# Optimization experiments

Measured on AMD Instinct MI355X. Metric: run time of the kernel, lower is better.

## Reference

```python
import jax, jax.numpy as jnp
import numpy as np

# geomloss SamplesLoss('sinkhorn', p=2, blur=0.05, diameter=4.0, scaling=0.5, debias=True)
P_EXP = 2.0
BLUR = 0.05
DIAMETER = 4.0
SCALING = 0.5


def eps_schedule():
    # geomloss epsilon_schedule: annealed temperatures from diameter^p down to blur^p
    mids = [np.exp(e) for e in np.arange(P_EXP * np.log(DIAMETER), P_EXP * np.log(BLUR), P_EXP * np.log(SCALING))]
    return [float(DIAMETER ** P_EXP)] + [float(e) for e in mids] + [float(BLUR ** P_EXP)]


def sq_cost(x, y):
    # C[b,i,j] = 0.5 * ||x_bi - y_bj||^2   (geomloss p=2 cost)
    x2 = jnp.sum(x * x, axis=-1)[:, :, None]   # [B,N,1]
    y2 = jnp.sum(y * y, axis=-1)[:, None, :]   # [B,1,M]
    return 0.5 * (x2 + y2) - jnp.einsum('bid,bjd->bij', x, y)


def softmin(eps, C, h):
    # h: [B,M] dual log-potential; C: [B,N,M] -> [B,N]
    return -eps * jax.nn.logsumexp(h[:, None, :] - C / eps, axis=2)


def sinkhorn_divergence(x, y):
    B, N, _ = x.shape
    M = y.shape[1]
    dt = x.dtype
    a_log = jnp.full((B, N), -np.log(N), dtype=dt)  # uniform weights (log)
    b_log = jnp.full((B, M), -np.log(M), dtype=dt)

    C_xy = sq_cost(x, y)
    C_yx = sq_cost(y, x)
    C_xx = sq_cost(x, x)
    C_yy = sq_cost(y, y)

    eps_list = eps_schedule()
    eps = eps_list[0]
    # initialization (damping = 1 for balanced OT)
    a_x = softmin(eps, C_xx, a_log)
    b_y = softmin(eps, C_yy, b_log)
    b_x = softmin(eps, C_xy, b_log)
    a_y = softmin(eps, C_yx, a_log)

    # eps-scaling descent with symmetrized updates (runs under no_grad in geomloss)
    for eps in eps_list:
        at_y = softmin(eps, C_yx, a_log + b_x / eps)
        bt_x = softmin(eps, C_xy, b_log + a_y / eps)
        at_x = softmin(eps, C_xx, a_log + a_x / eps)
        bt_y = softmin(eps, C_yy, b_log + b_y / eps)
        a_y, b_x = 0.5 * (a_y + at_y), 0.5 * (b_x + bt_x)
        a_x, b_y = 0.5 * (a_x + at_x), 0.5 * (b_y + bt_y)

    # last extrapolation: gradients flow only through the cost matrices here
    eps = eps_list[-1]
    sg = jax.lax.stop_gradient
    a_y, b_x = (softmin(eps, C_yx, sg(a_log + b_x / eps)),
                softmin(eps, C_xy, sg(b_log + a_y / eps)))
    a_x = softmin(eps, C_xx, sg(a_log + a_x / eps))
    b_y = softmin(eps, C_yy, sg(b_log + b_y / eps))

    a = jnp.exp(a_log)
    b = jnp.exp(b_log)
    # debiased Sinkhorn cost per batch, then torch.sum over batch as in forward()
    F = jnp.sum(a * (b_x - a_x), axis=-1) + jnp.sum(b * (a_y - b_y), axis=-1)
    return jnp.sum(F)


def setup_inputs() -> dict:
    key = jax.random.key(0)
    k1, k2 = jax.random.split(key)
    true_data = jax.random.normal(k1, (2, 4096, 3), dtype=jnp.float32)
    particles = jax.random.normal(k2, (2, 4096, 3), dtype=jnp.float32)
    return {"true_data": true_data, "particles": particles}


def reference(true_data, particles):
    # rm_map is identity here: y = rm_map(particles) = particles
    return sinkhorn_divergence(true_data, particles)
```

## Files before the change

### kernel.cpp

```cpp
#include <hip/hip_runtime.h>


typedef __attribute__((ext_vector_type(8))) short short8;
typedef __attribute__((ext_vector_type(8))) __bf16 bf16x8;
typedef __attribute__((ext_vector_type(4))) float f32x4;

#define NPT 4096
#define BLOCK 512
#define COLS 1024
#define NPARTS 4
#define ROWS_PER_BLOCK 256
#define NRC 16
#define EXP2 __builtin_amdgcn_exp2f
#define LOG2 __builtin_amdgcn_logf
#define KLOG2E 1.4426950408889634f
#define KLN2 0.6931471805599453f

__device__ inline unsigned short f2bf(float f) {
  unsigned u = __float_as_uint(f);
  return (unsigned short)((u + 0x7FFF + ((u >> 16) & 1)) >> 16);
}
__device__ inline float bf2f(unsigned short h) {
  return __uint_as_float(((unsigned)h) << 16);
}

struct SArgs {
  const float* rowPts[4];
  const float* colPts[4];
  const float2* Pprev;
  float2* Pcur;
  const float* Fprev;
  float* Fcur;
  float eps, epsPrev;
  int usePot, avgPrev;
};

__device__ inline void lse_merge8(float& m, float& s, f32x4 ca, f32x4 cb) {
  float cm = fmaxf(fmaxf(fmaxf(ca.x, ca.y), fmaxf(ca.z, ca.w)),
                   fmaxf(fmaxf(cb.x, cb.y), fmaxf(cb.z, cb.w)));
  float mn = fmaxf(m, cm);
  float sc = EXP2(m - mn);
  float cs = (EXP2(ca.x - mn) + EXP2(ca.y - mn)) + (EXP2(ca.z - mn) + EXP2(ca.w - mn))
           + (EXP2(cb.x - mn) + EXP2(cb.y - mn)) + (EXP2(cb.z - mn) + EXP2(cb.w - mn));
  s = fmaf(s, sc, cs);
  m = mn;
}

__global__ __launch_bounds__(BLOCK, 2) void softmin_mfma(SArgs A) {
  __shared__ short8 fragA0[COLS];
  __shared__ short8 fragA1[COLS];

  const int bid  = blockIdx.x;
  const int tbl  = bid >> 6;
  const int task = tbl >> 1, batch = tbl & 1;
  const int rem  = bid & 63;
  const int part = rem >> 4;
  const int rc   = rem & 15;

  const float* yp = A.colPts[task] + batch * NPT * 3;
  const float* xp = A.rowPts[task] + batch * NPT * 3;

  const float inv_eps = 1.0f / A.eps;
  const float sY = inv_eps * KLOG2E;
  const float hc = -8.317766166719343f;
  const int pidxA[4] = {1, 0, 2, 3};
  const int tP = pidxA[task] * 2 + batch;

  const int lane = threadIdx.x & 63;
  const int wave = threadIdx.x >> 6;
  const int q    = lane >> 4;

  const int rowbase = rc * ROWS_PER_BLOCK + wave * 32;
  bf16x8 Bf[2];
#pragma unroll
  for (int rs = 0; rs < 2; ++rs) {
    int i = rowbase + rs * 16 + (lane & 15);
    float X0 = xp[3 * i], X1 = xp[3 * i + 1], X2 = xp[3 * i + 2];
    unsigned short xh0 = f2bf(X0), xh1 = f2bf(X1), xh2 = f2bf(X2);
    unsigned short xl0 = f2bf(X0 - bf2f(xh0));
    unsigned short xl1 = f2bf(X1 - bf2f(xh1));
    unsigned short xl2 = f2bf(X2 - bf2f(xh2));
    short8 bb = (short8)0;
    if (q == 0) {
      short8 t = {(short)xh0, (short)xh1, (short)xh2,
                  (short)xh0, (short)xh1, (short)xh2,
                  (short)xl0, (short)xl1};
      bb = t;
    } else if (q == 1) {
      short8 t = {(short)xl2, (short)0x3F80, (short)0x3F80, (short)0x3F80,
                  (short)xl0, (short)xl1, (short)xl2, 0};
      bb = t;
    }
    Bf[rs] = __builtin_bit_cast(bf16x8, bb);
  }

  for (int c = 0; c < COLS / BLOCK; ++c) {
    int jl = threadIdx.x + c * BLOCK;
    int j  = part * COLS + jl;
    float y0 = yp[3 * j], y1 = yp[3 * j + 1], y2 = yp[3 * j + 2];
    float y2n = 0.5f * (y0 * y0 + y1 * y1 + y2 * y2);
    float pot = 0.0f;
    if (A.usePot) {
      float2 q0 = A.Pprev[(tP * 4 + 0) * NPT + j];
      float2 q1 = A.Pprev[(tP * 4 + 1) * NPT + j];
      float2 q2 = A.Pprev[(tP * 4 + 2) * NPT + j];
      float2 q3 = A.Pprev[(tP * 4 + 3) * NPT + j];
      float M = fmaxf(fmaxf(q0.x, q1.x), fmaxf(q2.x, q3.x));
      float S = q0.y * EXP2(q0.x - M) + q1.y * EXP2(q1.x - M)
              + q2.y * EXP2(q2.x - M) + q3.y * EXP2(q3.x - M);
      float L = M + LOG2(S);
      float r = y2n - A.epsPrev * KLN2 * L;
      if (A.avgPrev) r = 0.5f * (A.Fprev[tP * NPT + j] + r);
      pot = r;
      if (rc == 0) A.Fcur[tP * NPT + j] = pot;
    }
    float T = (hc + (pot - y2n) * inv_eps) * KLOG2E;
    float s0 = y0 * sY, s1 = y1 * sY, s2 = y2 * sY;
    unsigned short yh0 = f2bf(s0), yh1 = f2bf(s1), yh2 = f2bf(s2);
    unsigned short yl0 = f2bf(s0 - bf2f(yh0));
    unsigned short yl1 = f2bf(s1 - bf2f(yh1));
    unsigned short yl2 = f2bf(s2 - bf2f(yh2));
    unsigned short Th = f2bf(T);
    float tr = T - bf2f(Th);
    unsigned short Tm = f2bf(tr);
    tr -= bf2f(Tm);
    unsigned short Tl = f2bf(tr);
    short8 h0 = {(short)yh0, (short)yh1, (short)yh2,
                 (short)yl0, (short)yl1, (short)yl2,
                 (short)yh0, (short)yh1};
    short8 h1 = {(short)yh2, (short)Th, (short)Tm, (short)Tl,
                 (short)yl0, (short)yl1, (short)yl2, 0};
    fragA0[jl] = h0;
    fragA1[jl] = h1;
  }
  __syncthreads();

  const short8* srcA = (lane & 16) ? fragA1 : fragA0;
  const int colsel = lane & 15;
  const f32x4 Z = {0.0f, 0.0f, 0.0f, 0.0f};
  short8 a0s = (short8)0, a1s = (short8)0;
  float m0 = -__builtin_inff(), s0_ = 0.0f;
  float m1 = -__builtin_inff(), s1_ = 0.0f;

  for (int jt = 0; jt < COLS / 16; jt += 2) {
    if (lane < 32) {
      a0s = srcA[jt * 16 + colsel];
      a1s = srcA[jt * 16 + 16 + colsel];
    }
    bf16x8 A0 = __builtin_bit_cast(bf16x8, a0s);
    bf16x8 A1 = __builtin_bit_cast(bf16x8, a1s);
    f32x4 c00 = __builtin_amdgcn_mfma_f32_16x16x32_bf16(A0, Bf[0], Z, 0, 0, 0);
    f32x4 c10 = __builtin_amdgcn_mfma_f32_16x16x32_bf16(A1, Bf[0], Z, 0, 0, 0);
    f32x4 c01 = __builtin_amdgcn_mfma_f32_16x16x32_bf16(A0, Bf[1], Z, 0, 0, 0);
    f32x4 c11 = __builtin_amdgcn_mfma_f32_16x16x32_bf16(A1, Bf[1], Z, 0, 0, 0);
    lse_merge8(m0, s0_, c00, c10);
    lse_merge8(m1, s1_, c01, c11);
  }

#pragma unroll
  for (int rs = 0; rs < 2; ++rs) {
    float m = rs ? m1 : m0;
    float s = rs ? s1_ : s0_;
#pragma unroll
    for (int off = 16; off <= 32; off <<= 1) {
      float mo = __shfl_xor(m, off, 64);
      float so = __shfl_xor(s, off, 64);
      float mn = fmaxf(m, mo);
      s = s * EXP2(m - mn) + so * EXP2(mo - mn);
      m = mn;
    }
    if (lane < 16) {
      int i = rowbase + rs * 16 + lane;
      A.Pcur[(tbl * 4 + part) * NPT + i] = make_float2(m, s);
    }
  }
}

__global__ __launch_bounds__(256) void reduce1(const float2* P, float* R1) {
  int u = blockIdx.x * 256 + threadIdx.x;
  int b = u >> 12, i = u & 4095;
  float Ls[4];
#pragma unroll
  for (int t = 0; t < 4; ++t) {
    int tbl = t * 2 + b;
    float2 q0 = P[(tbl * 4 + 0) * NPT + i];
    float2 q1 = P[(tbl * 4 + 1) * NPT + i];
    float2 q2 = P[(tbl * 4 + 2) * NPT + i];
    float2 q3 = P[(tbl * 4 + 3) * NPT + i];
    float M = fmaxf(fmaxf(q0.x, q1.x), fmaxf(q2.x, q3.x));
    float S = q0.y * EXP2(q0.x - M) + q1.y * EXP2(q1.x - M)
            + q2.y * EXP2(q2.x - M) + q3.y * EXP2(q3.x - M);
    Ls[t] = M + LOG2(S);
  }
  float acc = (Ls[0] - Ls[2]) + (Ls[1] - Ls[3]);
#pragma unroll
  for (int off = 32; off >= 1; off >>= 1) acc += __shfl_xor(acc, off, 64);
  __shared__ float red[4];
  int wave = threadIdx.x >> 6, lane = threadIdx.x & 63;
  if (lane == 0) red[wave] = acc;
  __syncthreads();
  if (threadIdx.x == 0)
    R1[blockIdx.x] = red[0] + red[1] + red[2] + red[3];
}

__global__ __launch_bounds__(64) void reduce2(const float* R1, float* out) {
  float a = (threadIdx.x < 32) ? R1[threadIdx.x] : 0.0f;
#pragma unroll
  for (int off = 32; off >= 1; off >>= 1) a += __shfl_xor(a, off, 64);
  if (threadIdx.x == 0)
    out[0] = a * (-0.0025f * KLN2 / 4096.0f);
}

extern "C" void kernel_launch(void* const* d_in, const int* in_sizes, int n_in,
                              void* d_out, int out_size, void* d_ws, size_t ws_size,
                              hipStream_t stream) {
  const float* x = (const float*)d_in[0];
  const float* y = (const float*)d_in[1];
  float* out = (float*)d_out;
  float* W = (float*)d_ws;

  float2* P[2] = { (float2*)W, (float2*)(W + 262144) };
  float*  F[2] = { W + 524288, W + 557056 };
  float*  R1buf = W + 589824;

  static const float epsL[11] = {16.0f, 16.0f, 16.0f, 4.0f, 1.0f, 0.25f, 0.0625f,
                                 0.015625f, 0.00390625f, 0.0025f, 0.0025f};
  static const int avgL[11] = {0, 1, 1, 1, 1, 1, 1, 1, 1, 1, 0};

  const float* rows[4] = { x, y, x, y };
  const float* cols[4] = { y, x, x, y };

  dim3 grid(8 * NPARTS * NRC), block(BLOCK);
  for (int L = 0; L <= 10; ++L) {
    SArgs A;
    for (int t = 0; t < 4; ++t) { A.rowPts[t] = rows[t]; A.colPts[t] = cols[t]; }
    A.Pprev = P[(L + 1) & 1];
    A.Pcur  = P[L & 1];
    A.Fprev = F[(L + 1) & 1];
    A.Fcur  = F[L & 1];
    A.eps = epsL[L];
    A.epsPrev = (L > 0) ? epsL[L - 1] : 1.0f;
    A.usePot = (L > 0) ? 1 : 0;
    A.avgPrev = (L > 0) ? avgL[L - 1] : 0;
    softmin_mfma<<<grid, block, 0, stream>>>(A);
  }
  reduce1<<<32, 256, 0, stream>>>(P[0], R1buf);
  reduce2<<<1, 64, 0, stream>>>(R1buf, out);
}
```

Measured before the change: 365.4 us.

## Shrink softmin blocks, split columns into eight parts, remove lane-divergent LDS loads

Halves the block size, the columns per block and the rows per block, and doubles the number of column partitions. This gives four times as many blocks and allows up to 8 blocks per CU, which is meant to improve occupancy and latency hiding. The LDS fragment loads become unconditional: a zero-padded region and a zero stride serve the upper lanes, replacing the branch. The max and exp reductions are also restructured to use paired vectors. In exchange, the partial-LSE merges across more parts cost more, and the workspace buffers grow.

```diff
diff --git a/kernel.cpp b/kernel.cpp
--- a/kernel.cpp
+++ b/kernel.cpp
@@ -4,13 +4,14 @@
 typedef __attribute__((ext_vector_type(8))) short short8;
 typedef __attribute__((ext_vector_type(8))) __bf16 bf16x8;
 typedef __attribute__((ext_vector_type(4))) float f32x4;
+typedef __attribute__((ext_vector_type(2))) float f32x2;
 
 #define NPT 4096
-#define BLOCK 512
-#define COLS 1024
-#define NPARTS 4
-#define ROWS_PER_BLOCK 256
-#define NRC 16
+#define BLOCK 256
+#define COLS 512
+#define NPARTS 8
+#define ROWS_PER_BLOCK 128
+#define NRC 32
 #define EXP2 __builtin_amdgcn_exp2f
 #define LOG2 __builtin_amdgcn_logf
 #define KLOG2E 1.4426950408889634f
@@ -35,27 +36,33 @@
   int usePot, avgPrev;
 };
 
-__device__ inline void lse_merge8(float& m, float& s, f32x4 ca, f32x4 cb) {
-  float cm = fmaxf(fmaxf(fmaxf(ca.x, ca.y), fmaxf(ca.z, ca.w)),
-                   fmaxf(fmaxf(cb.x, cb.y), fmaxf(cb.z, cb.w)));
+__device__ inline void lse_merge8(float& m, float& s, f32x4 a, f32x4 b) {
+  float t0 = fmaxf(fmaxf(a.x, a.y), a.z);
+  float t1 = fmaxf(fmaxf(a.w, b.x), b.y);
+  float t2 = fmaxf(b.z, b.w);
+  float cm = fmaxf(fmaxf(t0, t1), t2);
   float mn = fmaxf(m, cm);
   float sc = EXP2(m - mn);
-  float cs = (EXP2(ca.x - mn) + EXP2(ca.y - mn)) + (EXP2(ca.z - mn) + EXP2(ca.w - mn))
-           + (EXP2(cb.x - mn) + EXP2(cb.y - mn)) + (EXP2(cb.z - mn) + EXP2(cb.w - mn));
-  s = fmaf(s, sc, cs);
+  f32x2 mn2 = {mn, mn};
+  f32x2 sa, sb, d;
+  d = (f32x2){a.x, a.y} - mn2; sa = (f32x2){EXP2(d.x), EXP2(d.y)};
+  d = (f32x2){a.z, a.w} - mn2; sb = (f32x2){EXP2(d.x), EXP2(d.y)};
+  d = (f32x2){b.x, b.y} - mn2; sa += (f32x2){EXP2(d.x), EXP2(d.y)};
+  d = (f32x2){b.z, b.w} - mn2; sb += (f32x2){EXP2(d.x), EXP2(d.y)};
+  sa += sb;
+  s = fmaf(s, sc, sa.x + sa.y);
   m = mn;
 }
 
-__global__ __launch_bounds__(BLOCK, 2) void softmin_mfma(SArgs A) {
-  __shared__ short8 fragA0[COLS];
-  __shared__ short8 fragA1[COLS];
+__global__ __launch_bounds__(BLOCK, 8) void softmin_mfma(SArgs A) {
+  __shared__ short8 frag[2 * COLS + 32];
 
   const int bid  = blockIdx.x;
-  const int tbl  = bid >> 6;
+  const int tbl  = bid >> 8;
   const int task = tbl >> 1, batch = tbl & 1;
-  const int rem  = bid & 63;
-  const int part = rem >> 4;
-  const int rc   = rem & 15;
+  const int rem  = bid & 255;
+  const int part = rem >> 5;
+  const int rc   = rem & 31;
 
   const float* yp = A.colPts[task] + batch * NPT * 3;
   const float* xp = A.rowPts[task] + batch * NPT * 3;
@@ -94,6 +101,8 @@
     Bf[rs] = __builtin_bit_cast(bf16x8, bb);
   }
 
+  if (threadIdx.x < 32) frag[2 * COLS + threadIdx.x] = (short8)0;
+
   for (int c = 0; c < COLS / BLOCK; ++c) {
     int jl = threadIdx.x + c * BLOCK;
     int j  = part * COLS + jl;
@@ -101,13 +110,16 @@
     float y2n = 0.5f * (y0 * y0 + y1 * y1 + y2 * y2);
     float pot = 0.0f;
     if (A.usePot) {
-      float2 q0 = A.Pprev[(tP * 4 + 0) * NPT + j];
-      float2 q1 = A.Pprev[(tP * 4 + 1) * NPT + j];
-      float2 q2 = A.Pprev[(tP * 4 + 2) * NPT + j];
-      float2 q3 = A.Pprev[(tP * 4 + 3) * NPT + j];
-      float M = fmaxf(fmaxf(q0.x, q1.x), fmaxf(q2.x, q3.x));
-      float S = q0.y * EXP2(q0.x - M) + q1.y * EXP2(q1.x - M)
-              + q2.y * EXP2(q2.x - M) + q3.y * EXP2(q3.x - M);
+      float M = -__builtin_inff();
+      float2 qv[NPARTS];
+#pragma unroll
+      for (int p = 0; p < NPARTS; ++p) {
+        qv[p] = A.Pprev[(tP * NPARTS + p) * NPT + j];
+        M = fmaxf(M, qv[p].x);
+      }
+      float S = 0.0f;
+#pragma unroll
+      for (int p = 0; p < NPARTS; ++p) S += qv[p].y * EXP2(qv[p].x - M);
       float L = M + LOG2(S);
       float r = y2n - A.epsPrev * KLN2 * L;
       if (A.avgPrev) r = 0.5f * (A.Fprev[tP * NPT + j] + r);
@@ -130,31 +142,30 @@
                  (short)yh0, (short)yh1};
     short8 h1 = {(short)yh2, (short)Th, (short)Tm, (short)Tl,
                  (short)yl0, (short)yl1, (short)yl2, 0};
-    fragA0[jl] = h0;
-    fragA1[jl] = h1;
+    frag[jl] = h0;
+    frag[COLS + jl] = h1;
   }
   __syncthreads();
 
-  const short8* srcA = (lane & 16) ? fragA1 : fragA0;
-  const int colsel = lane & 15;
-  const f32x4 Z = {0.0f, 0.0f, 0.0f, 0.0f};
-  short8 a0s = (short8)0, a1s = (short8)0;
+  int idx = ((q == 0) ? 0 : (q == 1) ? COLS : 2 * COLS) + (lane & 15);
+  const int stride = (lane < 32) ? 32 : 0;
   float m0 = -__builtin_inff(), s0_ = 0.0f;
   float m1 = -__builtin_inff(), s1_ = 0.0f;
 
-  for (int jt = 0; jt < COLS / 16; jt += 2) {
-    if (lane < 32) {
-      a0s = srcA[jt * 16 + colsel];
-      a1s = srcA[jt * 16 + 16 + colsel];
-    }
-    bf16x8 A0 = __builtin_bit_cast(bf16x8, a0s);
-    bf16x8 A1 = __builtin_bit_cast(bf16x8, a1s);
+#pragma unroll 4
+  for (int jt = 0; jt < COLS / 32; ++jt) {
+    short8 as0 = frag[idx];
+    short8 as1 = frag[idx + 16];
+    idx += stride;
+    bf16x8 A0 = __builtin_bit_cast(bf16x8, as0);
+    bf16x8 A1 = __builtin_bit_cast(bf16x8, as1);
+    const f32x4 Z = {0.0f, 0.0f, 0.0f, 0.0f};
     f32x4 c00 = __builtin_amdgcn_mfma_f32_16x16x32_bf16(A0, Bf[0], Z, 0, 0, 0);
-    f32x4 c10 = __builtin_amdgcn_mfma_f32_16x16x32_bf16(A1, Bf[0], Z, 0, 0, 0);
-    f32x4 c01 = __builtin_amdgcn_mfma_f32_16x16x32_bf16(A0, Bf[1], Z, 0, 0, 0);
+    f32x4 c01 = __builtin_amdgcn_mfma_f32_16x16x32_bf16(A1, Bf[0], Z, 0, 0, 0);
+    f32x4 c10 = __builtin_amdgcn_mfma_f32_16x16x32_bf16(A0, Bf[1], Z, 0, 0, 0);
     f32x4 c11 = __builtin_amdgcn_mfma_f32_16x16x32_bf16(A1, Bf[1], Z, 0, 0, 0);
-    lse_merge8(m0, s0_, c00, c10);
-    lse_merge8(m1, s1_, c01, c11);
+    lse_merge8(m0, s0_, c00, c01);
+    lse_merge8(m1, s1_, c10, c11);
   }
 
 #pragma unroll
@@ -171,7 +182,7 @@
     }
     if (lane < 16) {
       int i = rowbase + rs * 16 + lane;
-      A.Pcur[(tbl * 4 + part) * NPT + i] = make_float2(m, s);
+      A.Pcur[(tbl * NPARTS + part) * NPT + i] = make_float2(m, s);
     }
   }
 }
@@ -183,13 +194,16 @@
 #pragma unroll
   for (int t = 0; t < 4; ++t) {
     int tbl = t * 2 + b;
-    float2 q0 = P[(tbl * 4 + 0) * NPT + i];
-    float2 q1 = P[(tbl * 4 + 1) * NPT + i];
-    float2 q2 = P[(tbl * 4 + 2) * NPT + i];
-    float2 q3 = P[(tbl * 4 + 3) * NPT + i];
-    float M = fmaxf(fmaxf(q0.x, q1.x), fmaxf(q2.x, q3.x));
-    float S = q0.y * EXP2(q0.x - M) + q1.y * EXP2(q1.x - M)
-            + q2.y * EXP2(q2.x - M) + q3.y * EXP2(q3.x - M);
+    float M = -__builtin_inff();
+    float2 qv[NPARTS];
+#pragma unroll
+    for (int p = 0; p < NPARTS; ++p) {
+      qv[p] = P[(tbl * NPARTS + p) * NPT + i];
+      M = fmaxf(M, qv[p].x);
+    }
+    float S = 0.0f;
+#pragma unroll
+    for (int p = 0; p < NPARTS; ++p) S += qv[p].y * EXP2(qv[p].x - M);
     Ls[t] = M + LOG2(S);
   }
   float acc = (Ls[0] - Ls[2]) + (Ls[1] - Ls[3]);
@@ -219,9 +233,9 @@
   float* out = (float*)d_out;
   float* W = (float*)d_ws;
 
-  float2* P[2] = { (float2*)W, (float2*)(W + 262144) };
-  float*  F[2] = { W + 524288, W + 557056 };
-  float*  R1buf = W + 589824;
+  float2* P[2] = { (float2*)W, (float2*)(W + 524288) };
+  float*  F[2] = { W + 1048576, W + 1048576 + 32768 };
+  float*  R1buf = W + 1048576 + 65536;
 
   static const float epsL[11] = {16.0f, 16.0f, 16.0f, 4.0f, 1.0f, 0.25f, 0.0625f,
                                  0.015625f, 0.00390625f, 0.0025f, 0.0025f};
```

Result: no change. 364.4 us (-0.3%).

## Use 1024-thread blocks with one row tile per wave and zero-padded LDS fragments

Applied to the files above, without the earlier changes.

Doubles the block size so each wave handles 16 rows instead of 32, keeping one B fragment per wave and staging the column fragments with a single pass. The per-lane branch on LDS reads is replaced by a zero-padded region that upper-half lanes index with stride 0, and each iteration issues four MFMAs over 64 columns. The log-sum-exp merge now uses packed two-wide float max and subtract operations. This trades per-wave work and register use for more waves per block and fewer divergent loads, but every wave now reads the full column set from LDS, which doubles LDS traffic per row.

```diff
diff --git a/kernel.cpp b/kernel.cpp
--- a/kernel.cpp
+++ b/kernel.cpp
@@ -4,9 +4,10 @@
 typedef __attribute__((ext_vector_type(8))) short short8;
 typedef __attribute__((ext_vector_type(8))) __bf16 bf16x8;
 typedef __attribute__((ext_vector_type(4))) float f32x4;
+typedef __attribute__((ext_vector_type(2))) float f32x2;
 
 #define NPT 4096
-#define BLOCK 512
+#define BLOCK 1024
 #define COLS 1024
 #define NPARTS 4
 #define ROWS_PER_BLOCK 256
@@ -35,20 +36,39 @@
   int usePot, avgPrev;
 };
 
-__device__ inline void lse_merge8(float& m, float& s, f32x4 ca, f32x4 cb) {
-  float cm = fmaxf(fmaxf(fmaxf(ca.x, ca.y), fmaxf(ca.z, ca.w)),
-                   fmaxf(fmaxf(cb.x, cb.y), fmaxf(cb.z, cb.w)));
+__device__ inline void lse_merge16(float& m, float& s,
+                                   f32x4 c0, f32x4 c1, f32x4 c2, f32x4 c3) {
+  f32x2 p0 = {c0.x, c0.y}, p1 = {c0.z, c0.w};
+  f32x2 p2 = {c1.x, c1.y}, p3 = {c1.z, c1.w};
+  f32x2 p4 = {c2.x, c2.y}, p5 = {c2.z, c2.w};
+  f32x2 p6 = {c3.x, c3.y}, p7 = {c3.z, c3.w};
+  f32x2 q0 = __builtin_elementwise_max(p0, p1);
+  f32x2 q1 = __builtin_elementwise_max(p2, p3);
+  f32x2 q2 = __builtin_elementwise_max(p4, p5);
+  f32x2 q3 = __builtin_elementwise_max(p6, p7);
+  f32x2 r0 = __builtin_elementwise_max(q0, q1);
+  f32x2 r1 = __builtin_elementwise_max(q2, q3);
+  f32x2 rm = __builtin_elementwise_max(r0, r1);
+  float cm = fmaxf(rm.x, rm.y);
   float mn = fmaxf(m, cm);
   float sc = EXP2(m - mn);
-  float cs = (EXP2(ca.x - mn) + EXP2(ca.y - mn)) + (EXP2(ca.z - mn) + EXP2(ca.w - mn))
-           + (EXP2(cb.x - mn) + EXP2(cb.y - mn)) + (EXP2(cb.z - mn) + EXP2(cb.w - mn));
-  s = fmaf(s, sc, cs);
+  f32x2 mn2 = {mn, mn};
+  f32x2 sa, sb, d;
+  d = p0 - mn2; sa  = (f32x2){EXP2(d.x), EXP2(d.y)};
+  d = p1 - mn2; sb  = (f32x2){EXP2(d.x), EXP2(d.y)};
+  d = p2 - mn2; sa += (f32x2){EXP2(d.x), EXP2(d.y)};
+  d = p3 - mn2; sb += (f32x2){EXP2(d.x), EXP2(d.y)};
+  d = p4 - mn2; sa += (f32x2){EXP2(d.x), EXP2(d.y)};
+  d = p5 - mn2; sb += (f32x2){EXP2(d.x), EXP2(d.y)};
+  d = p6 - mn2; sa += (f32x2){EXP2(d.x), EXP2(d.y)};
+  d = p7 - mn2; sb += (f32x2){EXP2(d.x), EXP2(d.y)};
+  sa += sb;
+  s = fmaf(s, sc, sa.x + sa.y);
   m = mn;
 }
 
-__global__ __launch_bounds__(BLOCK, 2) void softmin_mfma(SArgs A) {
-  __shared__ short8 fragA0[COLS];
-  __shared__ short8 fragA1[COLS];
+__global__ __launch_bounds__(BLOCK, 8) void softmin_mfma(SArgs A) {
+  __shared__ short8 frag[2 * COLS + 64];
 
   const int bid  = blockIdx.x;
   const int tbl  = bid >> 6;
@@ -70,11 +90,10 @@
   const int wave = threadIdx.x >> 6;
   const int q    = lane >> 4;
 
-  const int rowbase = rc * ROWS_PER_BLOCK + wave * 32;
-  bf16x8 Bf[2];
-#pragma unroll
-  for (int rs = 0; rs < 2; ++rs) {
-    int i = rowbase + rs * 16 + (lane & 15);
+  const int rowbase = rc * ROWS_PER_BLOCK + wave * 16;
+  bf16x8 Bf;
+  {
+    int i = rowbase + (lane & 15);
     float X0 = xp[3 * i], X1 = xp[3 * i + 1], X2 = xp[3 * i + 2];
     unsigned short xh0 = f2bf(X0), xh1 = f2bf(X1), xh2 = f2bf(X2);
     unsigned short xl0 = f2bf(X0 - bf2f(xh0));
@@ -91,20 +110,22 @@
                   (short)xl0, (short)xl1, (short)xl2, 0};
       bb = t;
     }
-    Bf[rs] = __builtin_bit_cast(bf16x8, bb);
-  }
-
-  for (int c = 0; c < COLS / BLOCK; ++c) {
-    int jl = threadIdx.x + c * BLOCK;
+    Bf = __builtin_bit_cast(bf16x8, bb);
+  }
+
+  if (threadIdx.x < 64) frag[2 * COLS + threadIdx.x] = (short8)0;
+
+  {
+    int jl = threadIdx.x;
     int j  = part * COLS + jl;
     float y0 = yp[3 * j], y1 = yp[3 * j + 1], y2 = yp[3 * j + 2];
     float y2n = 0.5f * (y0 * y0 + y1 * y1 + y2 * y2);
     float pot = 0.0f;
     if (A.usePot) {
-      float2 q0 = A.Pprev[(tP * 4 + 0) * NPT + j];
-      float2 q1 = A.Pprev[(tP * 4 + 1) * NPT + j];
-      float2 q2 = A.Pprev[(tP * 4 + 2) * NPT + j];
-      float2 q3 = A.Pprev[(tP * 4 + 3) * NPT + j];
+      float2 q0 = A.Pprev[(tP * NPARTS + 0) * NPT + j];
+      float2 q1 = A.Pprev[(tP * NPARTS + 1) * NPT + j];
+      float2 q2 = A.Pprev[(tP * NPARTS + 2) * NPT + j];
+      float2 q3 = A.Pprev[(tP * NPARTS + 3) * NPT + j];
       float M = fmaxf(fmaxf(q0.x, q1.x), fmaxf(q2.x, q3.x));
       float S = q0.y * EXP2(q0.x - M) + q1.y * EXP2(q1.x - M)
               + q2.y * EXP2(q2.x - M) + q3.y * EXP2(q3.x - M);
@@ -130,37 +151,36 @@
                  (short)yh0, (short)yh1};
     short8 h1 = {(short)yh2, (short)Th, (short)Tm, (short)Tl,
                  (short)yl0, (short)yl1, (short)yl2, 0};
-    fragA0[jl] = h0;
-    fragA1[jl] = h1;
+    frag[jl] = h0;
+    frag[COLS + jl] = h1;
   }
   __syncthreads();
 
-  const short8* srcA = (lane & 16) ? fragA1 : fragA0;
-  const int colsel = lane & 15;
-  const f32x4 Z = {0.0f, 0.0f, 0.0f, 0.0f};
-  short8 a0s = (short8)0, a1s = (short8)0;
+  int idx = ((q == 0) ? 0 : (q == 1) ? COLS : 2 * COLS) + (lane & 15);
+  const int stride = (lane < 32) ? 64 : 0;
   float m0 = -__builtin_inff(), s0_ = 0.0f;
-  float m1 = -__builtin_inff(), s1_ = 0.0f;
-
-  for (int jt = 0; jt < COLS / 16; jt += 2) {
-    if (lane < 32) {
-      a0s = srcA[jt * 16 + colsel];
-      a1s = srcA[jt * 16 + 16 + colsel];
-    }
-    bf16x8 A0 = __builtin_bit_cast(bf16x8, a0s);
-    bf16x8 A1 = __builtin_bit_cast(bf16x8, a1s);
-    f32x4 c00 = __builtin_amdgcn_mfma_f32_16x16x32_bf16(A0, Bf[0], Z, 0, 0, 0);
-    f32x4 c10 = __builtin_amdgcn_mfma_f32_16x16x32_bf16(A1, Bf[0], Z, 0, 0, 0);
-    f32x4 c01 = __builtin_amdgcn_mfma_f32_16x16x32_bf16(A0, Bf[1], Z, 0, 0, 0);
-    f32x4 c11 = __builtin_amdgcn_mfma_f32_16x16x32_bf16(A1, Bf[1], Z, 0, 0, 0);
-    lse_merge8(m0, s0_, c00, c10);
-    lse_merge8(m1, s1_, c01, c11);
-  }
-
-#pragma unroll
-  for (int rs = 0; rs < 2; ++rs) {
-    float m = rs ? m1 : m0;
-    float s = rs ? s1_ : s0_;
+
+#pragma unroll 2
+  for (int jt = 0; jt < COLS / 64; ++jt) {
+    short8 as0 = frag[idx];
+    short8 as1 = frag[idx + 16];
+    short8 as2 = frag[idx + 32];
+    short8 as3 = frag[idx + 48];
+    idx += stride;
+    bf16x8 A0 = __builtin_bit_cast(bf16x8, as0);
+    bf16x8 A1 = __builtin_bit_cast(bf16x8, as1);
+    bf16x8 A2 = __builtin_bit_cast(bf16x8, as2);
+    bf16x8 A3 = __builtin_bit_cast(bf16x8, as3);
+    const f32x4 Z = {0.0f, 0.0f, 0.0f, 0.0f};
+    f32x4 c0 = __builtin_amdgcn_mfma_f32_16x16x32_bf16(A0, Bf, Z, 0, 0, 0);
+    f32x4 c1 = __builtin_amdgcn_mfma_f32_16x16x32_bf16(A1, Bf, Z, 0, 0, 0);
+    f32x4 c2 = __builtin_amdgcn_mfma_f32_16x16x32_bf16(A2, Bf, Z, 0, 0, 0);
+    f32x4 c3 = __builtin_amdgcn_mfma_f32_16x16x32_bf16(A3, Bf, Z, 0, 0, 0);
+    lse_merge16(m0, s0_, c0, c1, c2, c3);
+  }
+
+  {
+    float m = m0, s = s0_;
 #pragma unroll
     for (int off = 16; off <= 32; off <<= 1) {
       float mo = __shfl_xor(m, off, 64);
@@ -170,8 +190,8 @@
       m = mn;
     }
     if (lane < 16) {
-      int i = rowbase + rs * 16 + lane;
-      A.Pcur[(tbl * 4 + part) * NPT + i] = make_float2(m, s);
+      int i = rowbase + lane;
+      A.Pcur[(tbl * NPARTS + part) * NPT + i] = make_float2(m, s);
     }
   }
 }
@@ -183,10 +203,10 @@
 #pragma unroll
   for (int t = 0; t < 4; ++t) {
     int tbl = t * 2 + b;
-    float2 q0 = P[(tbl * 4 + 0) * NPT + i];
-    float2 q1 = P[(tbl * 4 + 1) * NPT + i];
-    float2 q2 = P[(tbl * 4 + 2) * NPT + i];
-    float2 q3 = P[(tbl * 4 + 3) * NPT + i];
+    float2 q0 = P[(tbl * NPARTS + 0) * NPT + i];
+    float2 q1 = P[(tbl * NPARTS + 1) * NPT + i];
+    float2 q2 = P[(tbl * NPARTS + 2) * NPT + i];
+    float2 q3 = P[(tbl * NPARTS + 3) * NPT + i];
     float M = fmaxf(fmaxf(q0.x, q1.x), fmaxf(q2.x, q3.x));
     float S = q0.y * EXP2(q0.x - M) + q1.y * EXP2(q1.x - M)
             + q2.y * EXP2(q2.x - M) + q3.y * EXP2(q3.x - M);
```

Measured after the change: 329.2 us. 1.11x faster.
